# Optimization experiments

Measured on AMD Instinct MI355X. Metric: run time of the kernel, lower is better.

Reference implementation:

```python
import jax, jax.numpy as jnp
import numpy as np

B, N, D = 512, 2048, 128
MASK_NEG = 1e30


def setup_inputs() -> dict:
    key = jax.random.key(0)
    ks = jax.random.split(key, 8)
    Q = jax.random.normal(ks[0], (B, D), dtype=jnp.float32)
    K = jax.random.normal(ks[1], (B, N, D), dtype=jnp.float32)
    V = jax.random.normal(ks[2], (B, N, D), dtype=jnp.float32)
    adj = jax.random.randint(ks[3], (B, N), 0, 2).astype(jnp.float32)  # 0/1 mask
    s_mask = jnp.zeros((B, N), dtype=jnp.int32)  # unused by forward, kept for fidelity
    # nn.Linear params (PyTorch default uniform init scale)
    bound = 1.0 / np.sqrt(D)
    W1 = jax.random.uniform(ks[4], (D, D), minval=-bound, maxval=bound, dtype=jnp.float32)
    b1 = jax.random.uniform(ks[5], (D,), minval=-bound, maxval=bound, dtype=jnp.float32)
    W2 = jax.random.uniform(ks[6], (D, D), minval=-bound, maxval=bound, dtype=jnp.float32)
    b2 = jax.random.uniform(ks[7], (D,), minval=-bound, maxval=bound, dtype=jnp.float32)
    return {"Q": Q, "K": K, "V": V, "adj": adj, "s_mask": s_mask,
            "W1": W1, "b1": b1, "W2": W2, "b2": b2}


def reference(Q, K, V, adj, s_mask, W1, b1, W2, b2):
    # linear1(Q): (B, D); linear2(K): (B, N, D)  (torch Linear: x @ W.T + b)
    Qp = Q @ W1.T + b1
    Kp = jnp.einsum('bnd,de->bne', K, W2.T) + b2
    # bmm(K, Q.unsqueeze(2)).permute -> (B, 1, N) attention logits
    alpha = jnp.einsum('bnd,bd->bn', Kp, Qp)
    alpha = alpha - (1.0 - adj) * 1e30  # mask_logic with adj
    attn_weight = jax.nn.softmax(alpha, axis=-1)  # (B, N)
    attn_sum = jnp.einsum('bn,bnd->bd', attn_weight, V)  # (B, D)
    return attn_weight[:, None, :], attn_sum
```

## Files before the change

### kernel.cpp

```cpp
#include <hip/hip_runtime.h>
#include <cmath>

#define BB 512
#define NN 2048
#define DD 128
#define SPLIT 4
#define NC (NN / SPLIT)

__global__ __launch_bounds__(128) void prep_kernel(
    const float* __restrict__ Q, const float* __restrict__ W1,
    const float* __restrict__ b1, const float* __restrict__ W2,
    const float* __restrict__ b2, float* __restrict__ qt,
    float* __restrict__ cvec) {
  const int b = blockIdx.x;
  const int t = threadIdx.x;
  __shared__ float Qs[DD];
  __shared__ float Qp[DD];
  __shared__ float red[DD];

  Qs[t] = Q[b * DD + t];
  __syncthreads();

  float acc = b1[t];
  const float4* w1row = (const float4*)(W1 + t * DD);
  #pragma unroll 8
  for (int i = 0; i < DD / 4; ++i) {
    float4 w = w1row[i];
    acc += Qs[4 * i + 0] * w.x + Qs[4 * i + 1] * w.y +
           Qs[4 * i + 2] * w.z + Qs[4 * i + 3] * w.w;
  }
  Qp[t] = acc;
  __syncthreads();

  float acc2 = 0.f;
  for (int e = 0; e < DD; ++e) acc2 += Qp[e] * W2[e * DD + t];
  qt[b * DD + t] = acc2;

  red[t] = Qp[t] * b2[t];
  __syncthreads();
  for (int s = 64; s > 0; s >>= 1) {
    if (t < s) red[t] += red[t + s];
    __syncthreads();
  }
  if (t == 0) cvec[b] = red[0];
}

__global__ __launch_bounds__(256, 8) void attn_part_kernel(
    const float* __restrict__ K, const float* __restrict__ V,
    const float* __restrict__ adj, const float* __restrict__ qt,
    const float* __restrict__ cvec, float* __restrict__ out_w,
    float* __restrict__ part, float* __restrict__ mloc,
    float* __restrict__ sloc) {
  const int b = blockIdx.x;
  const int sc = blockIdx.y;
  const int n0 = sc * NC;
  const int tid = threadIdx.x;
  const int sub = tid & 31;
  const int grp = tid >> 5;

  __shared__ float alpha[NC];
  __shared__ float redC[8 * DD];
  __shared__ float wredM[4];
  __shared__ float wredS[4];

  const float4 qv = ((const float4*)(qt + (size_t)b * DD))[sub];
  const float cb = cvec[b];
  const float4* K4 = (const float4*)(K + ((size_t)b * NN + n0) * DD);
  const float4* V4 = (const float4*)(V + ((size_t)b * NN + n0) * DD);
  const float* adjb = adj + (size_t)b * NN + n0;

  for (int nb = grp * 2; nb < NC; nb += 16) {
    float4 k0 = K4[(nb + 0) * 32 + sub];
    float4 k1 = K4[(nb + 1) * 32 + sub];
    float p0 = k0.x * qv.x + k0.y * qv.y + k0.z * qv.z + k0.w * qv.w;
    float p1 = k1.x * qv.x + k1.y * qv.y + k1.z * qv.z + k1.w * qv.w;
    #pragma unroll
    for (int off = 16; off > 0; off >>= 1) {
      p0 += __shfl_xor(p0, off);
      p1 += __shfl_xor(p1, off);
    }
    if (sub == 0) {
      alpha[nb + 0] = p0 + cb - (1.0f - adjb[nb + 0]) * 1e30f;
      alpha[nb + 1] = p1 + cb - (1.0f - adjb[nb + 1]) * 1e30f;
    }
  }
  __syncthreads();

  float m = -INFINITY;
  for (int i = tid; i < NC; i += 256) m = fmaxf(m, alpha[i]);
  #pragma unroll
  for (int off = 32; off > 0; off >>= 1) m = fmaxf(m, __shfl_xor(m, off));
  if ((tid & 63) == 0) wredM[tid >> 6] = m;
  __syncthreads();
  m = fmaxf(fmaxf(wredM[0], wredM[1]), fmaxf(wredM[2], wredM[3]));

  float s = 0.f;
  for (int i = tid; i < NC; i += 256) {
    float p = __expf(alpha[i] - m);
    alpha[i] = p;
    out_w[(size_t)b * NN + n0 + i] = p;
    s += p;
  }
  #pragma unroll
  for (int off = 32; off > 0; off >>= 1) s += __shfl_xor(s, off);
  if ((tid & 63) == 0) wredS[tid >> 6] = s;
  __syncthreads();
  s = wredS[0] + wredS[1] + wredS[2] + wredS[3];
  if (tid == 0) {
    mloc[b * SPLIT + sc] = m;
    sloc[b * SPLIT + sc] = s;
  }

  float ax = 0.f, ay = 0.f, az = 0.f, aw = 0.f;
  for (int nb = grp * 2; nb < NC; nb += 16) {
    float w0 = alpha[nb + 0];
    float w1 = alpha[nb + 1];
    float4 v0 = V4[(nb + 0) * 32 + sub];
    float4 v1 = V4[(nb + 1) * 32 + sub];
    ax += w0 * v0.x + w1 * v1.x;
    ay += w0 * v0.y + w1 * v1.y;
    az += w0 * v0.z + w1 * v1.z;
    aw += w0 * v0.w + w1 * v1.w;
  }
  float4 accv;
  accv.x = ax; accv.y = ay; accv.z = az; accv.w = aw;
  __syncthreads();
  ((float4*)redC)[grp * 32 + sub] = accv;
  __syncthreads();
  if (tid < DD) {
    float ssum = 0.f;
    #pragma unroll
    for (int g = 0; g < 8; ++g) ssum += redC[g * DD + tid];
    part[((size_t)b * SPLIT + sc) * DD + tid] = ssum;
  }
}

__global__ __launch_bounds__(256) void combine_kernel(
    const float* __restrict__ part, const float* __restrict__ mloc,
    const float* __restrict__ sloc, float* __restrict__ out_w,
    float* __restrict__ out_s) {
  const int b = blockIdx.x;
  const int tid = threadIdx.x;

  float M = -INFINITY;
  #pragma unroll
  for (int sc = 0; sc < SPLIT; ++sc) M = fmaxf(M, mloc[b * SPLIT + sc]);
  float f[SPLIT];
  float T = 0.f;
  #pragma unroll
  for (int sc = 0; sc < SPLIT; ++sc) {
    float e = __expf(mloc[b * SPLIT + sc] - M);
    T += sloc[b * SPLIT + sc] * e;
    f[sc] = e;
  }
  const float inv = 1.0f / T;
  #pragma unroll
  for (int sc = 0; sc < SPLIT; ++sc) f[sc] *= inv;

  if (tid < DD) {
    float acc = 0.f;
    #pragma unroll
    for (int sc = 0; sc < SPLIT; ++sc)
      acc += part[((size_t)b * SPLIT + sc) * DD + tid] * f[sc];
    out_s[(size_t)b * DD + tid] = acc;
  }

  float4* w4 = (float4*)(out_w + (size_t)b * NN);
  for (int i = tid; i < NN / 4; i += 256) {
    const float fs = f[i >> 7];
    float4 v = w4[i];
    v.x *= fs; v.y *= fs; v.z *= fs; v.w *= fs;
    w4[i] = v;
  }
}

extern "C" void kernel_launch(void* const* d_in, const int* in_sizes, int n_in,
                              void* d_out, int out_size, void* d_ws, size_t ws_size,
                              hipStream_t stream) {
  const float* Q   = (const float*)d_in[0];
  const float* K   = (const float*)d_in[1];
  const float* V   = (const float*)d_in[2];
  const float* adj = (const float*)d_in[3];
  const float* W1  = (const float*)d_in[5];
  const float* b1  = (const float*)d_in[6];
  const float* W2  = (const float*)d_in[7];
  const float* b2  = (const float*)d_in[8];

  float* out_w = (float*)d_out;
  float* out_s = out_w + (size_t)BB * NN;

  float* qt   = (float*)d_ws;
  float* cvec = qt + (size_t)BB * DD;
  float* part = cvec + BB;
  float* mloc = part + (size_t)BB * SPLIT * DD;
  float* sloc = mloc + (size_t)BB * SPLIT;

  prep_kernel<<<BB, DD, 0, stream>>>(Q, W1, b1, W2, b2, qt, cvec);
  dim3 grid2(BB, SPLIT);
  attn_part_kernel<<<grid2, 256, 0, stream>>>(K, V, adj, qt, cvec, out_w,
                                              part, mloc, sloc);
  combine_kernel<<<BB, 256, 0, stream>>>(part, mloc, sloc, out_w, out_s);
}
```

Baseline: 1.005 ms.

## Fuse logits, softmax and V accumulation into one online-softmax pass with prefetch

Replaces the three-phase attn_part kernel (logits into shared memory, block max/sum reductions, then a separate V pass) with a single loop. Each 32-lane group keeps a running max, sum and weighted V accumulator, and the next K, V and adj rows are software-prefetched into registers. Per-group statistics are then merged with exp rescaling, and the unnormalized weights are written from the stored logits. This removes two block barriers and lets K and V loads overlap. In exchange it adds extra exp and rescale work per row and raises register pressure under launch bounds of 256 with 8 blocks.

```diff
diff --git a/kernel.cpp b/kernel.cpp
--- a/kernel.cpp
+++ b/kernel.cpp
@@ -60,8 +60,8 @@
 
   __shared__ float alpha[NC];
   __shared__ float redC[8 * DD];
-  __shared__ float wredM[4];
-  __shared__ float wredS[4];
+  __shared__ float gm[8];
+  __shared__ float gs[8];
 
   const float4 qv = ((const float4*)(qt + (size_t)b * DD))[sub];
   const float cb = cvec[b];
@@ -69,9 +69,29 @@
   const float4* V4 = (const float4*)(V + ((size_t)b * NN + n0) * DD);
   const float* adjb = adj + (size_t)b * NN + n0;
 
-  for (int nb = grp * 2; nb < NC; nb += 16) {
-    float4 k0 = K4[(nb + 0) * 32 + sub];
-    float4 k1 = K4[(nb + 1) * 32 + sub];
+  float m = -1e30f;
+  float s = 0.f;
+  float ax = 0.f, ay = 0.f, az = 0.f, aw = 0.f;
+
+  const int NT = NC / 16;
+  int rb = grp * 2;
+
+  float4 k0 = K4[(rb + 0) * 32 + sub];
+  float4 k1 = K4[(rb + 1) * 32 + sub];
+  float4 v0 = V4[(rb + 0) * 32 + sub];
+  float4 v1 = V4[(rb + 1) * 32 + sub];
+  float a0 = adjb[rb + 0];
+  float a1 = adjb[rb + 1];
+
+  for (int t = 0; t < NT; ++t) {
+    const int rb2 = (t + 1 < NT) ? rb + 16 : rb;
+    float4 nk0 = K4[(rb2 + 0) * 32 + sub];
+    float4 nk1 = K4[(rb2 + 1) * 32 + sub];
+    float4 nv0 = V4[(rb2 + 0) * 32 + sub];
+    float4 nv1 = V4[(rb2 + 1) * 32 + sub];
+    float na0 = adjb[rb2 + 0];
+    float na1 = adjb[rb2 + 1];
+
     float p0 = k0.x * qv.x + k0.y * qv.y + k0.z * qv.z + k0.w * qv.w;
     float p1 = k1.x * qv.x + k1.y * qv.y + k1.z * qv.z + k1.w * qv.w;
     #pragma unroll
@@ -79,60 +99,59 @@
       p0 += __shfl_xor(p0, off);
       p1 += __shfl_xor(p1, off);
     }
+    const float al0 = p0 + cb - (1.0f - a0) * 1e30f;
+    const float al1 = p1 + cb - (1.0f - a1) * 1e30f;
     if (sub == 0) {
-      alpha[nb + 0] = p0 + cb - (1.0f - adjb[nb + 0]) * 1e30f;
-      alpha[nb + 1] = p1 + cb - (1.0f - adjb[nb + 1]) * 1e30f;
+      alpha[rb + 0] = al0;
+      alpha[rb + 1] = al1;
     }
-  }
-  __syncthreads();
-
-  float m = -INFINITY;
-  for (int i = tid; i < NC; i += 256) m = fmaxf(m, alpha[i]);
-  #pragma unroll
-  for (int off = 32; off > 0; off >>= 1) m = fmaxf(m, __shfl_xor(m, off));
-  if ((tid & 63) == 0) wredM[tid >> 6] = m;
-  __syncthreads();
-  m = fmaxf(fmaxf(wredM[0], wredM[1]), fmaxf(wredM[2], wredM[3]));
-
-  float s = 0.f;
-  for (int i = tid; i < NC; i += 256) {
-    float p = __expf(alpha[i] - m);
-    alpha[i] = p;
-    out_w[(size_t)b * NN + n0 + i] = p;
-    s += p;
-  }
-  #pragma unroll
-  for (int off = 32; off > 0; off >>= 1) s += __shfl_xor(s, off);
-  if ((tid & 63) == 0) wredS[tid >> 6] = s;
-  __syncthreads();
-  s = wredS[0] + wredS[1] + wredS[2] + wredS[3];
-  if (tid == 0) {
-    mloc[b * SPLIT + sc] = m;
-    sloc[b * SPLIT + sc] = s;
-  }
-
-  float ax = 0.f, ay = 0.f, az = 0.f, aw = 0.f;
-  for (int nb = grp * 2; nb < NC; nb += 16) {
-    float w0 = alpha[nb + 0];
-    float w1 = alpha[nb + 1];
-    float4 v0 = V4[(nb + 0) * 32 + sub];
-    float4 v1 = V4[(nb + 1) * 32 + sub];
-    ax += w0 * v0.x + w1 * v1.x;
-    ay += w0 * v0.y + w1 * v1.y;
-    az += w0 * v0.z + w1 * v1.z;
-    aw += w0 * v0.w + w1 * v1.w;
-  }
+
+    const float mnew = fmaxf(m, fmaxf(al0, al1));
+    const float scale = __expf(m - mnew);
+    m = mnew;
+    const float e0 = __expf(al0 - m);
+    const float e1 = __expf(al1 - m);
+    s = s * scale + (e0 + e1);
+    ax = ax * scale + e0 * v0.x + e1 * v1.x;
+    ay = ay * scale + e0 * v0.y + e1 * v1.y;
+    az = az * scale + e0 * v0.z + e1 * v1.z;
+    aw = aw * scale + e0 * v0.w + e1 * v1.w;
+
+    k0 = nk0; k1 = nk1; v0 = nv0; v1 = nv1; a0 = na0; a1 = na1;
+    rb = rb2;
+  }
+
+  if (sub == 0) { gm[grp] = m; gs[grp] = s; }
   float4 accv;
   accv.x = ax; accv.y = ay; accv.z = az; accv.w = aw;
-  __syncthreads();
   ((float4*)redC)[grp * 32 + sub] = accv;
   __syncthreads();
+
+  float M = gm[0];
+  #pragma unroll
+  for (int g = 1; g < 8; ++g) M = fmaxf(M, gm[g]);
+  float fg[8];
+  float S = 0.f;
+  #pragma unroll
+  for (int g = 0; g < 8; ++g) {
+    fg[g] = __expf(gm[g] - M);
+    S += gs[g] * fg[g];
+  }
+
+  if (tid == 0) {
+    mloc[b * SPLIT + sc] = M;
+    sloc[b * SPLIT + sc] = S;
+  }
+
   if (tid < DD) {
     float ssum = 0.f;
     #pragma unroll
-    for (int g = 0; g < 8; ++g) ssum += redC[g * DD + tid];
+    for (int g = 0; g < 8; ++g) ssum += redC[g * DD + tid] * fg[g];
     part[((size_t)b * SPLIT + sc) * DD + tid] = ssum;
   }
+
+  for (int i = tid; i < NC; i += 256)
+    out_w[(size_t)b * NN + n0 + i] = __expf(alpha[i] - M);
 }
 
 __global__ __launch_bounds__(256) void combine_kernel(
```

New measurement: 1.018 ms. About the same (+1.3%).
